# Kernel optimization log

Measured on AMD Instinct MI355X. Metric: run time of the kernel, lower is better.

## Reference

```python
import jax, jax.numpy as jnp
import numpy as np

N = 50000
E = 800000
NEG_SLOPE = 0.2


def gat_layer(x, src, dst, W, al, ar):
    # x: [N, F_in]; W: [F_in, H*D]; al/ar: [H, D]
    H, D = al.shape
    feat = (x @ W).reshape(N, H, D)                      # [N, H, D]
    el = jnp.einsum('nhd,hd->nh', feat, al)              # [N, H]
    er = jnp.einsum('nhd,hd->nh', feat, ar)              # [N, H]
    e = jax.nn.leaky_relu(el[src] + er[dst], NEG_SLOPE)  # [E, H]
    # segment softmax over edges grouped by destination node
    m = jax.ops.segment_max(e, dst, num_segments=N)      # [N, H] (-inf for empty)
    a = jnp.exp(e - m[dst])                              # [E, H]
    s = jax.ops.segment_sum(a, dst, num_segments=N)      # [N, H]
    a = a / jnp.where(s[dst] > 0, s[dst], 1.0)
    # weighted gather-aggregate of messages
    out = jax.ops.segment_sum(a[:, :, None] * feat[src], dst, num_segments=N)
    return out                                           # [N, H, D]


def setup_inputs() -> dict:
    key = jax.random.key(0)
    ks = jax.random.split(key, 9)
    in_size, hid, out_size = 512, 64, 64
    H1, H2 = 4, 4
    return {
        'x':   jax.random.normal(ks[0], (N, in_size), dtype=jnp.float32),
        'src': jax.random.randint(ks[1], (E,), 0, N, dtype=jnp.int32),
        'dst': jax.random.randint(ks[2], (E,), 0, N, dtype=jnp.int32),
        'W1':  jax.random.normal(ks[3], (in_size, H1 * hid), dtype=jnp.float32) * 0.05,
        'al1': jax.random.normal(ks[4], (H1, hid), dtype=jnp.float32) * 0.1,
        'ar1': jax.random.normal(ks[5], (H1, hid), dtype=jnp.float32) * 0.1,
        'W2':  jax.random.normal(ks[6], (H1 * hid, H2 * out_size), dtype=jnp.float32) * 0.05,
        'al2': jax.random.normal(ks[7], (H2, out_size), dtype=jnp.float32) * 0.1,
        'ar2': jax.random.normal(ks[8], (H2, out_size), dtype=jnp.float32) * 0.1,
    }


def reference(x, src, dst, W1, al1, ar1, W2, al2, ar2):
    h = gat_layer(x, src, dst, W1, al1, ar1)   # [N, H1, hid]
    h = jax.nn.elu(h).reshape(N, -1)           # flatten heads -> [N, H1*hid]
    h = gat_layer(h, src, dst, W2, al2, ar2)   # [N, H2, out]
    return h.mean(axis=1)                      # mean over heads -> [N, out]
```

## Files before the change

kernel.cpp:

```cpp
#include <hip/hip_runtime.h>

#define NNODES 50000
#define NEDGES 800000
#define HH 4
#define DD 64
#define FEAT 256
#define NB ((NNODES + 255) / 256)
#define MPAD 50048

typedef __attribute__((ext_vector_type(8))) _Float16 frag16;
typedef __attribute__((ext_vector_type(4))) float frag_cd;
typedef __attribute__((ext_vector_type(4))) _Float16 h4v;

__global__ __launch_bounds__(256) void prep_kernel(
    const float* __restrict__ x, const float* __restrict__ W1,
    const float* __restrict__ W2, _Float16* __restrict__ Ap,
    _Float16* __restrict__ Bp1, _Float16* __restrict__ Bp2, int M) {
  int b = blockIdx.x;
  if (b < MPAD / 2) {
    int id = b * 256 + threadIdx.x;
    int m = id >> 7;
    int k4 = (id & 127) << 2;
    float4 v = make_float4(0.f, 0.f, 0.f, 0.f);
    if (m < M) v = *(const float4*)&x[(size_t)m * 512 + k4];
    h4v o;
    o[0] = (_Float16)v.x; o[1] = (_Float16)v.y;
    o[2] = (_Float16)v.z; o[3] = (_Float16)v.w;
    *(h4v*)&Ap[(size_t)m * 512 + k4] = o;
  } else {
    int idx = (b - MPAD / 2) * 256 + threadIdx.x;
    if (idx < 512 * 256) {
      int k = idx >> 8, n = idx & 255;
      Bp1[(size_t)n * 512 + k] = (_Float16)W1[idx];
    } else {
      idx -= 512 * 256;
      int k = idx >> 8, n = idx & 255;
      Bp2[(size_t)n * 256 + k] = (_Float16)W2[idx];
    }
  }
}

__global__ __launch_bounds__(256) void mfma_gemm_kernel(
    const _Float16* __restrict__ Ap, const _Float16* __restrict__ Bp,
    _Float16* __restrict__ featb, const float* __restrict__ al,
    const float* __restrict__ ar, float* __restrict__ elp,
    float* __restrict__ erp, int M, int K) {
  __shared__ _Float16 As[128 * 64];
  __shared__ _Float16 Bs[128 * 64];
  const int tid = threadIdx.x;
  const int w = tid >> 6, lane = tid & 63;
  const int q = lane >> 4, ln = lane & 15;
  const int rowBase = blockIdx.x * 128;
  const int colBase = blockIdx.y * 128;
  const int wm = (w >> 1) * 64;
  const int wn = (w & 1) * 64;

  frag_cd acc[4][4] = {};

  const int i1 = K >> 6;
  const int srow8 = lane >> 3;
  const int scg = ((lane & 7) ^ srow8) * 8;
  const int sw = ln & 7;

  for (int it = 0; it < i1; ++it) {
    const int kk = it << 6;
    __syncthreads();
#pragma unroll
    for (int j = 0; j < 4; ++j) {
      int rloc = w * 32 + j * 8 + srow8;
      __builtin_amdgcn_global_load_lds(
          (const __attribute__((address_space(1))) void*)(Ap + (size_t)(rowBase + rloc) * K + kk + scg),
          (__attribute__((address_space(3))) void*)(&As[(w * 32 + j * 8) * 64 + lane * 8]), 16, 0, 0);
    }
#pragma unroll
    for (int j = 0; j < 4; ++j) {
      int rloc = w * 32 + j * 8 + srow8;
      __builtin_amdgcn_global_load_lds(
          (const __attribute__((address_space(1))) void*)(Bp + (size_t)(colBase + rloc) * K + kk + scg),
          (__attribute__((address_space(3))) void*)(&Bs[(w * 32 + j * 8) * 64 + lane * 8]), 16, 0, 0);
    }
    __syncthreads();

#pragma unroll
    for (int ksub = 0; ksub < 2; ++ksub) {
      const int slot = ((ksub * 4 + q) ^ sw) * 8;
      frag16 a[4], b[4];
#pragma unroll
      for (int i = 0; i < 4; ++i)
        a[i] = *(const frag16*)&As[(wm + i * 16 + ln) * 64 + slot];
#pragma unroll
      for (int j = 0; j < 4; ++j)
        b[j] = *(const frag16*)&Bs[(wn + j * 16 + ln) * 64 + slot];
#pragma unroll
      for (int i = 0; i < 4; ++i)
#pragma unroll
        for (int j = 0; j < 4; ++j)
          acc[i][j] = __builtin_amdgcn_mfma_f32_16x16x32_f16(a[i], b[j], acc[i][j], 0, 0, 0);
    }
  }

#pragma unroll
  for (int i = 0; i < 4; ++i) {
    int rowg = rowBase + wm + i * 16 + q * 4;
#pragma unroll
    for (int r = 0; r < 4; ++r) {
      int row = rowg + r;
      if (row < M) {
#pragma unroll
        for (int j = 0; j < 4; ++j) {
          int col = colBase + wn + j * 16 + ln;
          featb[(size_t)row * 256 + col] = (_Float16)acc[i][j][r];
        }
      }
    }
  }

  const int h = (colBase + wn) >> 6;
  float alv[4], arv[4];
#pragma unroll
  for (int j = 0; j < 4; ++j) {
    alv[j] = al[h * DD + j * 16 + ln];
    arv[j] = ar[h * DD + j * 16 + ln];
  }
#pragma unroll
  for (int i = 0; i < 4; ++i) {
#pragma unroll
    for (int r = 0; r < 4; ++r) {
      float pl = 0.f, pr = 0.f;
#pragma unroll
      for (int j = 0; j < 4; ++j) {
        pl = fmaf(acc[i][j][r], alv[j], pl);
        pr = fmaf(acc[i][j][r], arv[j], pr);
      }
#pragma unroll
      for (int msk = 1; msk < 16; msk <<= 1) {
        pl += __shfl_xor(pl, msk);
        pr += __shfl_xor(pr, msk);
      }
      int row = rowBase + wm + i * 16 + q * 4 + r;
      if (ln == 0 && row < M) {
        elp[row * HH + h] = pl;
        erp[row * HH + h] = pr;
      }
    }
  }
}

__global__ __launch_bounds__(256) void hist_kernel(const int* __restrict__ dst,
                                                   int* __restrict__ deg) {
  int e = blockIdx.x * 256 + threadIdx.x;
  if (e < NEDGES) atomicAdd(&deg[dst[e]], 1);
}

__global__ __launch_bounds__(256) void scan_block_kernel(const int* __restrict__ deg,
                                                         int* __restrict__ off,
                                                         int* __restrict__ bsum) {
  __shared__ int tmp[256];
  int b = blockIdx.x, t = threadIdx.x;
  int i = b * 256 + t;
  int v = (i < NNODES) ? deg[i] : 0;
  tmp[t] = v;
  __syncthreads();
  for (int s = 1; s < 256; s <<= 1) {
    int add = (t >= s) ? tmp[t - s] : 0;
    __syncthreads();
    tmp[t] += add;
    __syncthreads();
  }
  if (i < NNODES) off[i + 1] = tmp[t];
  if (t == 255) bsum[b] = tmp[255];
}

__global__ __launch_bounds__(256) void scan_top_kernel(int* __restrict__ bsum) {
  __shared__ int tmp[256];
  int t = threadIdx.x;
  int v = (t < NB) ? bsum[t] : 0;
  tmp[t] = v;
  __syncthreads();
  for (int s = 1; s < 256; s <<= 1) {
    int add = (t >= s) ? tmp[t - s] : 0;
    __syncthreads();
    tmp[t] += add;
    __syncthreads();
  }
  if (t < NB) bsum[t] = tmp[t] - v;
}

__global__ __launch_bounds__(256) void scan_add_kernel(int* __restrict__ off,
                                                       const int* __restrict__ bsum,
                                                       int* __restrict__ cursor) {
  int b = blockIdx.x, t = threadIdx.x;
  int i = b * 256 + t;
  if (i < NNODES) {
    int val = off[i + 1] + bsum[b];
    off[i + 1] = val;
    if (i + 1 < NNODES) cursor[i + 1] = val;
  }
  if (i == 0) { off[0] = 0; cursor[0] = 0; }
}

__global__ __launch_bounds__(256) void scatter_kernel(const int* __restrict__ src,
                                                      const int* __restrict__ dst,
                                                      int* __restrict__ cursor,
                                                      int* __restrict__ csr_src) {
  int e = blockIdx.x * 256 + threadIdx.x;
  if (e >= NEDGES) return;
  int d = dst[e];
  int pos = atomicAdd(&cursor[d], 1);
  csr_src[pos] = src[e];
}

template <int LAYER>
__global__ __launch_bounds__(256) void gat_agg_kernel(
    const int* __restrict__ off, const int* __restrict__ csr_src,
    const float* __restrict__ el, const float* __restrict__ er,
    const _Float16* __restrict__ featb, float* __restrict__ outp,
    _Float16* __restrict__ outs) {
  __shared__ float sA[4][HH][68];
  __shared__ int sS[4][64];
  const int w = threadIdx.x >> 6;
  const int lane = threadIdx.x & 63;
  const int n = blockIdx.x * 4 + w;
  const int beg = off[n];
  const int deg = off[n + 1] - beg;

  float4 accv = make_float4(0.f, 0.f, 0.f, 0.f);
  const int h2 = lane >> 4;
  const int cb = lane << 2;

  if (deg > 0 && deg <= 64) {
    const int h1 = lane & 3, j1 = lane >> 2;
    const float erd = er[n * HH + h1];
    float e[4], a[4];
    float m = -INFINITY;
#pragma unroll
    for (int p = 0; p < 4; ++p) {
      int j = j1 + p * 16;
      float ev = -INFINITY;
      if (j < deg) {
        int s = csr_src[beg + j];
        if (h1 == 0) sS[w][j] = s;
        ev = el[s * HH + h1] + erd;
        ev = ev > 0.f ? ev : 0.2f * ev;
      }
      e[p] = ev;
      m = fmaxf(m, ev);
    }
#pragma unroll
    for (int msk = 4; msk <= 32; msk <<= 1) m = fmaxf(m, __shfl_xor(m, msk));
    float ps = 0.f;
#pragma unroll
    for (int p = 0; p < 4; ++p) {
      a[p] = (j1 + p * 16 < deg) ? __expf(e[p] - m) : 0.f;
      ps += a[p];
    }
#pragma unroll
    for (int msk = 4; msk <= 32; msk <<= 1) ps += __shfl_xor(ps, msk);
    const float sinv = 1.f / ps;
#pragma unroll
    for (int p = 0; p < 4; ++p) {
      int j = j1 + p * 16;
      if (j < deg) sA[w][h1][j] = a[p] * sinv;
    }

    int j = 0;
    for (; j + 4 <= deg; j += 4) {
      int s0 = sS[w][j], s1 = sS[w][j + 1], s2 = sS[w][j + 2], s3 = sS[w][j + 3];
      float a0 = sA[w][h2][j], a1 = sA[w][h2][j + 1];
      float a2 = sA[w][h2][j + 2], a3 = sA[w][h2][j + 3];
      h4v u0 = *(const h4v*)&featb[(size_t)s0 * FEAT + cb];
      h4v u1 = *(const h4v*)&featb[(size_t)s1 * FEAT + cb];
      h4v u2 = *(const h4v*)&featb[(size_t)s2 * FEAT + cb];
      h4v u3 = *(const h4v*)&featb[(size_t)s3 * FEAT + cb];
      accv.x = fmaf(a0, (float)u0[0], accv.x); accv.y = fmaf(a0, (float)u0[1], accv.y);
      accv.z = fmaf(a0, (float)u0[2], accv.z); accv.w = fmaf(a0, (float)u0[3], accv.w);
      accv.x = fmaf(a1, (float)u1[0], accv.x); accv.y = fmaf(a1, (float)u1[1], accv.y);
      accv.z = fmaf(a1, (float)u1[2], accv.z); accv.w = fmaf(a1, (float)u1[3], accv.w);
      accv.x = fmaf(a2, (float)u2[0], accv.x); accv.y = fmaf(a2, (float)u2[1], accv.y);
      accv.z = fmaf(a2, (float)u2[2], accv.z); accv.w = fmaf(a2, (float)u2[3], accv.w);
      accv.x = fmaf(a3, (float)u3[0], accv.x); accv.y = fmaf(a3, (float)u3[1], accv.y);
      accv.z = fmaf(a3, (float)u3[2], accv.z); accv.w = fmaf(a3, (float)u3[3], accv.w);
    }
    for (; j < deg; ++j) {
      int s0 = sS[w][j];
      float a0 = sA[w][h2][j];
      h4v u0 = *(const h4v*)&featb[(size_t)s0 * FEAT + cb];
      accv.x = fmaf(a0, (float)u0[0], accv.x); accv.y = fmaf(a0, (float)u0[1], accv.y);
      accv.z = fmaf(a0, (float)u0[2], accv.z); accv.w = fmaf(a0, (float)u0[3], accv.w);
    }
  } else if (deg > 64) {
    const int h1 = lane & 3, j1 = lane >> 2;
    const float erd = er[n * HH + h1];
    float m = -INFINITY;
    for (int j = j1; j < deg; j += 16) {
      int s = csr_src[beg + j];
      float ev = el[s * HH + h1] + erd;
      ev = ev > 0.f ? ev : 0.2f * ev;
      m = fmaxf(m, ev);
    }
#pragma unroll
    for (int msk = 4; msk <= 32; msk <<= 1) m = fmaxf(m, __shfl_xor(m, msk));
    float ps = 0.f;
    for (int j = j1; j < deg; j += 16) {
      int s = csr_src[beg + j];
      float ev = el[s * HH + h1] + erd;
      ev = ev > 0.f ? ev : 0.2f * ev;
      ps += __expf(ev - m);
    }
#pragma unroll
    for (int msk = 4; msk <= 32; msk <<= 1) ps += __shfl_xor(ps, msk);
    const float m2 = __shfl(m, h2);
    const float psinv2 = 1.f / __shfl(ps, h2);
    const float erd2 = er[n * HH + h2];
    for (int j = 0; j < deg; ++j) {
      int s = csr_src[beg + j];
      float ev = el[s * HH + h2] + erd2;
      ev = ev > 0.f ? ev : 0.2f * ev;
      float a0 = __expf(ev - m2) * psinv2;
      h4v u0 = *(const h4v*)&featb[(size_t)s * FEAT + cb];
      accv.x = fmaf(a0, (float)u0[0], accv.x); accv.y = fmaf(a0, (float)u0[1], accv.y);
      accv.z = fmaf(a0, (float)u0[2], accv.z); accv.w = fmaf(a0, (float)u0[3], accv.w);
    }
  }

  if (LAYER == 1) {
    float vv[4] = {accv.x, accv.y, accv.z, accv.w};
    h4v o;
#pragma unroll
    for (int c = 0; c < 4; ++c) {
      float v = vv[c];
      v = v > 0.f ? v : (__expf(v) - 1.f);
      o[c] = (_Float16)v;
    }
    *(h4v*)&outs[(size_t)n * 256 + cb] = o;
  } else {
#pragma unroll
    for (int msk = 16; msk <= 32; msk <<= 1) {
      accv.x += __shfl_xor(accv.x, msk);
      accv.y += __shfl_xor(accv.y, msk);
      accv.z += __shfl_xor(accv.z, msk);
      accv.w += __shfl_xor(accv.w, msk);
    }
    if (lane < 16) {
      float4 o = make_float4(0.25f * accv.x, 0.25f * accv.y,
                             0.25f * accv.z, 0.25f * accv.w);
      *(float4*)&outp[(size_t)n * DD + (lane << 2)] = o;
    }
  }
}

extern "C" void kernel_launch(void* const* d_in, const int* in_sizes, int n_in,
                              void* d_out, int out_size, void* d_ws, size_t ws_size,
                              hipStream_t stream) {
  const float* x   = (const float*)d_in[0];
  const int*   src = (const int*)d_in[1];
  const int*   dst = (const int*)d_in[2];
  const float* W1  = (const float*)d_in[3];
  const float* al1 = (const float*)d_in[4];
  const float* ar1 = (const float*)d_in[5];
  const float* W2  = (const float*)d_in[6];
  const float* al2 = (const float*)d_in[7];
  const float* ar2 = (const float*)d_in[8];
  float* out = (float*)d_out;

  float* ws = (float*)d_ws;
  float* el = ws;
  float* er = el + NNODES * HH;
  int* deg     = (int*)(er + NNODES * HH);
  int* off     = deg + NNODES;
  int* cursor  = off + NNODES + 1;
  int* bsum    = cursor + NNODES;
  int* csr_src = bsum + 256;
  uintptr_t p = ((uintptr_t)(csr_src + NEDGES) + 63) & ~(uintptr_t)63;
  _Float16* featb = (_Float16*)p;
  _Float16* Apr = featb + (size_t)NNODES * 256;
  Apr = (_Float16*)(((uintptr_t)Apr + 63) & ~(uintptr_t)63);
  _Float16* Bpr1 = Apr + (size_t)MPAD * 512;
  _Float16* Bpr2 = Bpr1 + 256 * 512;

  const int edgeBlocks = (NEDGES + 255) / 256;
  dim3 mfmaGrid(MPAD / 128, 2);

  hipMemsetAsync(deg, 0, NNODES * sizeof(int), stream);
  hist_kernel<<<edgeBlocks, 256, 0, stream>>>(dst, deg);
  scan_block_kernel<<<NB, 256, 0, stream>>>(deg, off, bsum);
  scan_top_kernel<<<1, 256, 0, stream>>>(bsum);
  scan_add_kernel<<<NB, 256, 0, stream>>>(off, bsum, cursor);
  scatter_kernel<<<edgeBlocks, 256, 0, stream>>>(src, dst, cursor, csr_src);

  prep_kernel<<<MPAD / 2 + 768, 256, 0, stream>>>(x, W1, W2, Apr, Bpr1, Bpr2, NNODES);

  mfma_gemm_kernel<<<mfmaGrid, 256, 0, stream>>>(Apr, Bpr1, featb, al1, ar1, el, er, NNODES, 512);
  gat_agg_kernel<1><<<NNODES / 4, 256, 0, stream>>>(off, csr_src, el, er, featb, nullptr, Apr);

  mfma_gemm_kernel<<<mfmaGrid, 256, 0, stream>>>(Apr, Bpr2, featb, al2, ar2, el, er, NNODES, 256);
  gat_agg_kernel<2><<<NNODES / 4, 256, 0, stream>>>(off, csr_src, el, er, featb, out, nullptr);
}
```

Baseline: 436.5 us.

## Split GAT aggregation into score pass and feature-sliced gather kernels

Splits aggregation into two kernels. A score kernel writes normalized fp16 attention weights per edge and head. A slice-gather kernel reads features stored in eight 32-column slices so each block's working set is smaller and more cache-friendly. Source indices are packed to 16-bit, which fits N=50000 since it is below 65536. Layer-2 head averaging now uses atomicAdd into a zeroed output, and the change adds extra kernel launches, an edge-weight array round trip, and atomic traffic.

```diff
diff --git a/kernel.cpp b/kernel.cpp
--- a/kernel.cpp
+++ b/kernel.cpp
@@ -7,6 +7,7 @@
 #define FEAT 256
 #define NB ((NNODES + 255) / 256)
 #define MPAD 50048
+#define SLSTRIDE ((size_t)NNODES * 32)
 
 typedef __attribute__((ext_vector_type(8))) _Float16 frag16;
 typedef __attribute__((ext_vector_type(4))) float frag_cd;
@@ -109,7 +110,8 @@
 #pragma unroll
         for (int j = 0; j < 4; ++j) {
           int col = colBase + wn + j * 16 + ln;
-          featb[(size_t)row * 256 + col] = (_Float16)acc[i][j][r];
+          featb[(size_t)(col >> 5) * SLSTRIDE + (size_t)row * 32 + (col & 31)] =
+              (_Float16)acc[i][j][r];
         }
       }
     }
@@ -202,35 +204,26 @@
 __global__ __launch_bounds__(256) void scatter_kernel(const int* __restrict__ src,
                                                       const int* __restrict__ dst,
                                                       int* __restrict__ cursor,
-                                                      int* __restrict__ csr_src) {
+                                                      unsigned short* __restrict__ csr16) {
   int e = blockIdx.x * 256 + threadIdx.x;
   if (e >= NEDGES) return;
   int d = dst[e];
   int pos = atomicAdd(&cursor[d], 1);
-  csr_src[pos] = src[e];
-}
-
-template <int LAYER>
-__global__ __launch_bounds__(256) void gat_agg_kernel(
-    const int* __restrict__ off, const int* __restrict__ csr_src,
+  csr16[pos] = (unsigned short)src[e];
+}
+
+__global__ __launch_bounds__(256) void score_kernel(
+    const int* __restrict__ off, const unsigned short* __restrict__ csr16,
     const float* __restrict__ el, const float* __restrict__ er,
-    const _Float16* __restrict__ featb, float* __restrict__ outp,
-    _Float16* __restrict__ outs) {
-  __shared__ float sA[4][HH][68];
-  __shared__ int sS[4][64];
-  const int w = threadIdx.x >> 6;
-  const int lane = threadIdx.x & 63;
+    _Float16* __restrict__ wa) {
+  const int w = threadIdx.x >> 6, lane = threadIdx.x & 63;
   const int n = blockIdx.x * 4 + w;
   const int beg = off[n];
   const int deg = off[n + 1] - beg;
-
-  float4 accv = make_float4(0.f, 0.f, 0.f, 0.f);
-  const int h2 = lane >> 4;
-  const int cb = lane << 2;
-
-  if (deg > 0 && deg <= 64) {
-    const int h1 = lane & 3, j1 = lane >> 2;
-    const float erd = er[n * HH + h1];
+  if (deg <= 0) return;
+  const int h1 = lane & 3, j1 = lane >> 2;
+  const float erd = er[n * HH + h1];
+  if (deg <= 64) {
     float e[4], a[4];
     float m = -INFINITY;
 #pragma unroll
@@ -238,8 +231,7 @@
       int j = j1 + p * 16;
       float ev = -INFINITY;
       if (j < deg) {
-        int s = csr_src[beg + j];
-        if (h1 == 0) sS[w][j] = s;
+        int s = csr16[beg + j];
         ev = el[s * HH + h1] + erd;
         ev = ev > 0.f ? ev : 0.2f * ev;
       }
@@ -260,40 +252,12 @@
 #pragma unroll
     for (int p = 0; p < 4; ++p) {
       int j = j1 + p * 16;
-      if (j < deg) sA[w][h1][j] = a[p] * sinv;
-    }
-
-    int j = 0;
-    for (; j + 4 <= deg; j += 4) {
-      int s0 = sS[w][j], s1 = sS[w][j + 1], s2 = sS[w][j + 2], s3 = sS[w][j + 3];
-      float a0 = sA[w][h2][j], a1 = sA[w][h2][j + 1];
-      float a2 = sA[w][h2][j + 2], a3 = sA[w][h2][j + 3];
-      h4v u0 = *(const h4v*)&featb[(size_t)s0 * FEAT + cb];
-      h4v u1 = *(const h4v*)&featb[(size_t)s1 * FEAT + cb];
-      h4v u2 = *(const h4v*)&featb[(size_t)s2 * FEAT + cb];
-      h4v u3 = *(const h4v*)&featb[(size_t)s3 * FEAT + cb];
-      accv.x = fmaf(a0, (float)u0[0], accv.x); accv.y = fmaf(a0, (float)u0[1], accv.y);
-      accv.z = fmaf(a0, (float)u0[2], accv.z); accv.w = fmaf(a0, (float)u0[3], accv.w);
-      accv.x = fmaf(a1, (float)u1[0], accv.x); accv.y = fmaf(a1, (float)u1[1], accv.y);
-      accv.z = fmaf(a1, (float)u1[2], accv.z); accv.w = fmaf(a1, (float)u1[3], accv.w);
-      accv.x = fmaf(a2, (float)u2[0], accv.x); accv.y = fmaf(a2, (float)u2[1], accv.y);
-      accv.z = fmaf(a2, (float)u2[2], accv.z); accv.w = fmaf(a2, (float)u2[3], accv.w);
-      accv.x = fmaf(a3, (float)u3[0], accv.x); accv.y = fmaf(a3, (float)u3[1], accv.y);
-      accv.z = fmaf(a3, (float)u3[2], accv.z); accv.w = fmaf(a3, (float)u3[3], accv.w);
-    }
-    for (; j < deg; ++j) {
-      int s0 = sS[w][j];
-      float a0 = sA[w][h2][j];
-      h4v u0 = *(const h4v*)&featb[(size_t)s0 * FEAT + cb];
-      accv.x = fmaf(a0, (float)u0[0], accv.x); accv.y = fmaf(a0, (float)u0[1], accv.y);
-      accv.z = fmaf(a0, (float)u0[2], accv.z); accv.w = fmaf(a0, (float)u0[3], accv.w);
-    }
-  } else if (deg > 64) {
-    const int h1 = lane & 3, j1 = lane >> 2;
-    const float erd = er[n * HH + h1];
+      if (j < deg) wa[(size_t)h1 * NEDGES + beg + j] = (_Float16)(a[p] * sinv);
+    }
+  } else {
     float m = -INFINITY;
     for (int j = j1; j < deg; j += 16) {
-      int s = csr_src[beg + j];
+      int s = csr16[beg + j];
       float ev = el[s * HH + h1] + erd;
       ev = ev > 0.f ? ev : 0.2f * ev;
       m = fmaxf(m, ev);
@@ -302,50 +266,88 @@
     for (int msk = 4; msk <= 32; msk <<= 1) m = fmaxf(m, __shfl_xor(m, msk));
     float ps = 0.f;
     for (int j = j1; j < deg; j += 16) {
-      int s = csr_src[beg + j];
+      int s = csr16[beg + j];
       float ev = el[s * HH + h1] + erd;
       ev = ev > 0.f ? ev : 0.2f * ev;
       ps += __expf(ev - m);
     }
 #pragma unroll
     for (int msk = 4; msk <= 32; msk <<= 1) ps += __shfl_xor(ps, msk);
-    const float m2 = __shfl(m, h2);
-    const float psinv2 = 1.f / __shfl(ps, h2);
-    const float erd2 = er[n * HH + h2];
-    for (int j = 0; j < deg; ++j) {
-      int s = csr_src[beg + j];
-      float ev = el[s * HH + h2] + erd2;
+    const float sinv = 1.f / ps;
+    for (int j = j1; j < deg; j += 16) {
+      int s = csr16[beg + j];
+      float ev = el[s * HH + h1] + erd;
       ev = ev > 0.f ? ev : 0.2f * ev;
-      float a0 = __expf(ev - m2) * psinv2;
-      h4v u0 = *(const h4v*)&featb[(size_t)s * FEAT + cb];
-      accv.x = fmaf(a0, (float)u0[0], accv.x); accv.y = fmaf(a0, (float)u0[1], accv.y);
-      accv.z = fmaf(a0, (float)u0[2], accv.z); accv.w = fmaf(a0, (float)u0[3], accv.w);
-    }
-  }
-
+      wa[(size_t)h1 * NEDGES + beg + j] = (_Float16)(__expf(ev - m) * sinv);
+    }
+  }
+}
+
+template <int LAYER>
+__global__ __launch_bounds__(256) void slice_gather_kernel(
+    const int* __restrict__ off, const unsigned short* __restrict__ csr16,
+    const _Float16* __restrict__ wa, const _Float16* __restrict__ featb,
+    float* __restrict__ outp, _Float16* __restrict__ outs) {
+  const int w = threadIdx.x >> 6, lane = threadIdx.x & 63;
+  const int sl = blockIdx.x & 7;
+  const int nb = blockIdx.x >> 3;
+  const int node_sub = lane >> 3, fsub = lane & 7;
+  const int n = nb * 32 + w * 8 + node_sub;
+  const int h = sl >> 1;
+  const _Float16* __restrict__ fp = featb + (size_t)sl * SLSTRIDE;
+  const _Float16* __restrict__ wap = wa + (size_t)h * NEDGES;
+
+  int beg = 0, deg = 0;
+  if (n < NNODES) { beg = off[n]; deg = off[n + 1] - beg; }
+  int md = deg;
+#pragma unroll
+  for (int msk = 8; msk <= 32; msk <<= 1) md = max(md, __shfl_xor(md, msk));
+
+  float acc[4] = {0.f, 0.f, 0.f, 0.f};
+  for (int jb = 0; jb < md; jb += 64) {
+    int sv[8];
+    float wv[8];
+#pragma unroll
+    for (int t = 0; t < 8; ++t) {
+      int e = jb + t * 8 + fsub;
+      sv[t] = 0;
+      wv[t] = 0.f;
+      if (e < deg) {
+        sv[t] = __builtin_nontemporal_load(&csr16[beg + e]);
+        wv[t] = (float)__builtin_nontemporal_load(&wap[beg + e]);
+      }
+    }
+#pragma unroll
+    for (int t = 0; t < 8; ++t) {
+      if (jb + t * 8 >= md) break;
+#pragma unroll
+      for (int k = 0; k < 8; ++k) {
+        int s = __shfl(sv[t], (node_sub << 3) | k);
+        float a = __shfl(wv[t], (node_sub << 3) | k);
+        h4v u = *(const h4v*)&fp[(size_t)s * 32 + (fsub << 2)];
+        acc[0] = fmaf(a, (float)u[0], acc[0]);
+        acc[1] = fmaf(a, (float)u[1], acc[1]);
+        acc[2] = fmaf(a, (float)u[2], acc[2]);
+        acc[3] = fmaf(a, (float)u[3], acc[3]);
+      }
+    }
+  }
+
+  if (n >= NNODES) return;
   if (LAYER == 1) {
-    float vv[4] = {accv.x, accv.y, accv.z, accv.w};
     h4v o;
 #pragma unroll
     for (int c = 0; c < 4; ++c) {
-      float v = vv[c];
+      float v = acc[c];
       v = v > 0.f ? v : (__expf(v) - 1.f);
       o[c] = (_Float16)v;
     }
-    *(h4v*)&outs[(size_t)n * 256 + cb] = o;
+    *(h4v*)&outs[(size_t)n * 256 + sl * 32 + (fsub << 2)] = o;
   } else {
-#pragma unroll
-    for (int msk = 16; msk <= 32; msk <<= 1) {
-      accv.x += __shfl_xor(accv.x, msk);
-      accv.y += __shfl_xor(accv.y, msk);
-      accv.z += __shfl_xor(accv.z, msk);
-      accv.w += __shfl_xor(accv.w, msk);
-    }
-    if (lane < 16) {
-      float4 o = make_float4(0.25f * accv.x, 0.25f * accv.y,
-                             0.25f * accv.z, 0.25f * accv.w);
-      *(float4*)&outp[(size_t)n * DD + (lane << 2)] = o;
-    }
+    const int dbase = (sl & 1) * 32 + (fsub << 2);
+#pragma unroll
+    for (int c = 0; c < 4; ++c)
+      atomicAdd(&outp[(size_t)n * DD + dbase + c], 0.25f * acc[c]);
   }
 }
 
@@ -370,29 +372,34 @@
   int* off     = deg + NNODES;
   int* cursor  = off + NNODES + 1;
   int* bsum    = cursor + NNODES;
-  int* csr_src = bsum + 256;
-  uintptr_t p = ((uintptr_t)(csr_src + NEDGES) + 63) & ~(uintptr_t)63;
+  unsigned short* csr16 = (unsigned short*)(bsum + 256);
+  _Float16* wa = (_Float16*)(csr16 + NEDGES);
+  uintptr_t p = ((uintptr_t)(wa + (size_t)4 * NEDGES) + 63) & ~(uintptr_t)63;
   _Float16* featb = (_Float16*)p;
-  _Float16* Apr = featb + (size_t)NNODES * 256;
+  _Float16* Apr = featb + (size_t)8 * SLSTRIDE;
   Apr = (_Float16*)(((uintptr_t)Apr + 63) & ~(uintptr_t)63);
   _Float16* Bpr1 = Apr + (size_t)MPAD * 512;
   _Float16* Bpr2 = Bpr1 + 256 * 512;
 
   const int edgeBlocks = (NEDGES + 255) / 256;
   dim3 mfmaGrid(MPAD / 128, 2);
+  const int gatGrid = ((NNODES + 31) / 32) * 8;
 
   hipMemsetAsync(deg, 0, NNODES * sizeof(int), stream);
+  hipMemsetAsync(out, 0, (size_t)NNODES * DD * sizeof(float), stream);
   hist_kernel<<<edgeBlocks, 256, 0, stream>>>(dst, deg);
   scan_block_kernel<<<NB, 256, 0, stream>>>(deg, off, bsum);
   scan_top_kernel<<<1, 256, 0, stream>>>(bsum);
   scan_add_kernel<<<NB, 256, 0, stream>>>(off, bsum, cursor);
-  scatter_kernel<<<edgeBlocks, 256, 0, stream>>>(src, dst, cursor, csr_src);
+  scatter_kernel<<<edgeBlocks, 256, 0, stream>>>(src, dst, cursor, csr16);
 
   prep_kernel<<<MPAD / 2 + 768, 256, 0, stream>>>(x, W1, W2, Apr, Bpr1, Bpr2, NNODES);
 
   mfma_gemm_kernel<<<mfmaGrid, 256, 0, stream>>>(Apr, Bpr1, featb, al1, ar1, el, er, NNODES, 512);
-  gat_agg_kernel<1><<<NNODES / 4, 256, 0, stream>>>(off, csr_src, el, er, featb, nullptr, Apr);
+  score_kernel<<<NNODES / 4, 256, 0, stream>>>(off, csr16, el, er, wa);
+  slice_gather_kernel<1><<<gatGrid, 256, 0, stream>>>(off, csr16, wa, featb, nullptr, Apr);
 
   mfma_gemm_kernel<<<mfmaGrid, 256, 0, stream>>>(Apr, Bpr2, featb, al2, ar2, el, er, NNODES, 256);
-  gat_agg_kernel<2><<<NNODES / 4, 256, 0, stream>>>(off, csr_src, el, er, featb, out, nullptr);
-}
+  score_kernel<<<NNODES / 4, 256, 0, stream>>>(off, csr16, el, er, wa);
+  slice_gather_kernel<2><<<gatGrid, 256, 0, stream>>>(off, csr16, wa, featb, out, nullptr);
+}
```

New measurement: 591.3 us. +35.5%, slower.
